# Optimization experiments

Hardware: AMD Instinct MI355X
Metric: run time of the kernel (lower is better)

Reference implementation:

```python
import jax, jax.numpy as jnp
import numpy as np

N = 20000      # nodes
E = 500000     # edges (~25 neighbors/node)
G = 64         # graphs in batch
NF = 64        # num_features (node dim)
NG = 100       # num_gaussians (edge dim)
L = 6          # conv layers
FC = 128       # fc_feat_size
NFC = 3        # num_fc_layers - 1
EMB = 92       # KHOT embedding width
CUTOFF = 6.0
EPS = 1e-5


def setup_inputs() -> dict:
    key = jax.random.key(0)
    ks = jax.random.split(key, 16)
    s = 0.05
    inp = {}
    inp['atomic_numbers'] = jax.random.randint(ks[0], (N,), 0, 100, dtype=jnp.int32)
    inp['neighbors_index'] = jax.random.randint(ks[1], (2, E), 0, N, dtype=jnp.int32)
    inp['distances'] = jax.random.uniform(ks[2], (E,), dtype=jnp.float32) * CUTOFF
    inp['batch'] = jnp.sort(jax.random.randint(ks[3], (N,), 0, G, dtype=jnp.int32))
    # parameters
    inp['embedding'] = jax.random.normal(ks[4], (100, EMB), jnp.float32) * s
    inp['nuc_W'] = jax.random.normal(ks[5], (EMB, NF), jnp.float32) * s
    inp['nuc_b'] = jnp.zeros((NF,), jnp.float32)
    inp['conv_W'] = jax.random.normal(ks[6], (L, 2 * NF + NG, 2 * NF), jnp.float32) * s
    inp['conv_b'] = jnp.zeros((L, 2 * NF), jnp.float32)
    inp['bn_g'] = jnp.ones((L, 2 * NF), jnp.float32)
    inp['bn_b'] = jnp.zeros((L, 2 * NF), jnp.float32)
    inp['ln_g'] = jnp.ones((L, NF), jnp.float32)
    inp['ln_b'] = jnp.zeros((L, NF), jnp.float32)
    inp['fc1_W'] = jax.random.normal(ks[7], (NF, FC), jnp.float32) * s
    inp['fc1_b'] = jnp.zeros((FC,), jnp.float32)
    inp['fcs_W'] = jax.random.normal(ks[8], (NFC, FC, FC), jnp.float32) * s
    inp['fcs_b'] = jnp.zeros((NFC, FC), jnp.float32)
    inp['out_W'] = jax.random.normal(ks[9], (FC, 1), jnp.float32) * s
    inp['out_b'] = jnp.zeros((1,), jnp.float32)
    return inp


def reference(atomic_numbers, neighbors_index, distances, batch,
              embedding, nuc_W, nuc_b, conv_W, conv_b, bn_g, bn_b,
              ln_g, ln_b, fc1_W, fc1_b, fcs_W, fcs_b, out_W, out_b):
    # Gaussian smearing of edge distances -> [E, NG]
    offsets = jnp.linspace(0.0, CUTOFF, NG)
    coeff = -0.5 / (offsets[1] - offsets[0]) ** 2
    ef = jnp.exp(coeff * (distances[:, None] - offsets) ** 2)

    # atom k-hot embedding -> nuclear linear embedding: [N, NF]
    x = embedding[atomic_numbers] @ nuc_W + nuc_b

    src, dst = neighbors_index[0], neighbors_index[1]  # x_j = src, x_i = dst

    for l in range(L):
        # edge message: gather + concat + linear
        z = jnp.concatenate([x[dst], x[src], ef], axis=1) @ conv_W[l] + conv_b[l]
        # BatchNorm1d over edges (training-mode batch statistics, biased var)
        mu = z.mean(axis=0)
        var = jnp.mean((z - mu) ** 2, axis=0)
        z = (z - mu) / jnp.sqrt(var + EPS) * bn_g[l] + bn_b[l]
        z1, z2 = jnp.split(z, 2, axis=1)
        m = jax.nn.sigmoid(z1) * jax.nn.softplus(z2)  # [E, NF]
        # scatter-add aggregate to target nodes
        agg = jax.ops.segment_sum(m, dst, num_segments=N)
        # LayerNorm + residual + softplus
        mu2 = agg.mean(axis=-1, keepdims=True)
        var2 = jnp.mean((agg - mu2) ** 2, axis=-1, keepdims=True)
        h = (agg - mu2) / jnp.sqrt(var2 + EPS) * ln_g[l] + ln_b[l]
        x = jax.nn.softplus(h + x)

    # mean pool per graph
    counts = jnp.maximum(jax.ops.segment_sum(jnp.ones((N,), x.dtype), batch, num_segments=G), 1.0)
    mol = jax.ops.segment_sum(x, batch, num_segments=G) / counts[:, None]

    h = jax.nn.softplus(mol @ fc1_W + fc1_b)
    for i in range(NFC):
        h = jax.nn.softplus(h @ fcs_W[i] + fcs_b[i])
    y = h @ out_W + out_b  # [G, 1]
    return y
```

## Files before the change

kernel.cpp:

```cpp
#include <hip/hip_runtime.h>
#include <hip/hip_fp16.h>
#include <cmath>

#define NN 20000
#define EE 500000
#define GG 64
#define TS 8192
#define SW 4096
#define EPS 1e-5f
#define LOG2E 1.442695040888963f
#define LN2 0.693147180559945f

typedef unsigned long long u64a __attribute__((aligned(4)));
typedef _Float16 f16x8 __attribute__((ext_vector_type(8)));
typedef float f32x4 __attribute__((ext_vector_type(4)));

__device__ __forceinline__ float softplus_ref(float x) {
    return fmaxf(x, 0.f) + log1pf(__expf(-fabsf(x)));
}
__device__ __forceinline__ float sigmoid_fast(float x) {
    return __builtin_amdgcn_rcpf(1.0f + __expf(-x));
}

__global__ void k_gtab(float* __restrict__ g) {
    int i = blockIdx.x * 256 + threadIdx.x;
    if (i >= TS * 100) return;
    int s = i / 100, k = i - 100 * s;
    float d = s * (6.0f / (TS - 1.0f));
    float o = k * (6.0f / 99.0f);
    float step = 6.0f / 99.0f;
    float coeff = -0.5f / (step * step);
    float df = d - o;
    g[i] = __expf(coeff * df * df);
}

__global__ void __launch_bounds__(256) k_build_T(
    const float* __restrict__ g, const float* __restrict__ convW,
    const float* __restrict__ convB, __half2* __restrict__ Tn) {
    int lane = threadIdx.x & 63;
    int wv = __builtin_amdgcn_readfirstlane(threadIdx.x >> 6);
    int l = blockIdx.y;
    int s0 = blockIdx.x * 16 + wv * 4;
    const float* w = convW + ((size_t)l * 228 + 128) * 128;
    const float* g0 = g + (size_t)s0 * 100;
    float b0 = convB[l * 128 + lane], b1 = convB[l * 128 + lane + 64];
    float2 a0 = {b0, b1}, a1 = {b0, b1}, a2 = {b0, b1}, a3 = {b0, b1};
#pragma unroll 4
    for (int k = 0; k < 100; k++) {
        float w0 = w[k * 128 + lane];
        float w1 = w[k * 128 + lane + 64];
        float ga = g0[k], gb = g0[100 + k], gc = g0[200 + k], gd = g0[300 + k];
        a0.x += ga * w0; a0.y += ga * w1;
        a1.x += gb * w0; a1.y += gb * w1;
        a2.x += gc * w0; a2.y += gc * w1;
        a3.x += gd * w0; a3.y += gd * w1;
    }
    Tn[((size_t)l * TS + s0 + 0) * 64 + lane] = __floats2half2_rn(a0.x, a0.y);
    Tn[((size_t)l * TS + s0 + 1) * 64 + lane] = __floats2half2_rn(a1.x, a1.y);
    Tn[((size_t)l * TS + s0 + 2) * 64 + lane] = __floats2half2_rn(a2.x, a2.y);
    Tn[((size_t)l * TS + s0 + 3) * 64 + lane] = __floats2half2_rn(a3.x, a3.y);
}

__global__ void k_prepW2(const float* __restrict__ convW, _Float16* __restrict__ Wf) {
    int lane = threadIdx.x;
    int ct = blockIdx.x;
    int half = blockIdx.y;
    int l = blockIdx.z;
    int p = ct * 16 + (lane & 15);
    int s = p >> 7;
    int r = p & 127;
    int colW = (r >> 1) + (r & 1) * 64;
    int k0 = half * 32 + (lane >> 4) * 8;
    _Float16* dst = Wf + (((size_t)(l * 16 + ct) * 2 + half) * 64 + lane) * 8;
#pragma unroll
    for (int i = 0; i < 8; i++) {
        float v = convW[((size_t)l * 228 + s * 64 + k0 + i) * 128 + colW];
        dst[i] = (_Float16)v;
    }
}

__global__ void k_embed(const int* __restrict__ an, const float* __restrict__ emb,
                        const float* __restrict__ W, const float* __restrict__ b,
                        float* __restrict__ x, _Float16* __restrict__ xh) {
    int c = threadIdx.x & 63, nl = threadIdx.x >> 6;
    int n = blockIdx.x * 4 + nl;
    if (n >= NN) return;
    const float* e = emb + (size_t)an[n] * 92;
    float acc = b[c];
#pragma unroll 4
    for (int k = 0; k < 92; k++) acc += e[k] * W[k * 64 + c];
    x[(size_t)n * 64 + c] = acc;
    xh[(size_t)n * 64 + c] = (_Float16)acc;
}

__global__ void k_hist(const int* __restrict__ dst, int* __restrict__ counts) {
    int e = blockIdx.x * 256 + threadIdx.x;
    if (e < EE) atomicAdd(&counts[dst[e]], 1);
}

__global__ void k_scan_local(const int* __restrict__ counts, int* __restrict__ rp,
                             int* __restrict__ bsum) {
    __shared__ int buf[1024];
    int b = blockIdx.x, tid = threadIdx.x;
    int i = b * 1024 + tid;
    int val = (i < NN) ? counts[i] : 0;
    buf[tid] = val;
    __syncthreads();
    for (int off = 1; off < 1024; off <<= 1) {
        int t = (tid >= off) ? buf[tid - off] : 0;
        __syncthreads();
        buf[tid] += t;
        __syncthreads();
    }
    if (i < NN) rp[i + 1] = buf[tid];
    if (tid == 1023) bsum[b] = buf[1023];
}

__global__ void k_scan_off(int* __restrict__ bsum, int nb) {
    if (threadIdx.x == 0) {
        int acc = 0;
        for (int b = 0; b < nb; b++) { int v = bsum[b]; bsum[b] = acc; acc += v; }
    }
}

__global__ void k_scan_add(int* __restrict__ rp, const int* __restrict__ bsum) {
    int b = blockIdx.x, tid = threadIdx.x;
    int i = b * 1024 + tid;
    if (i < NN) rp[i + 1] += bsum[b];
    if (b == 0 && tid == 0) rp[0] = 0;
}

__global__ void k_wsn(const int* __restrict__ rp, int* __restrict__ wsn) {
    int w = blockIdx.x * 256 + threadIdx.x;
    if (w >= SW) return;
    int e0 = (int)((long long)w * EE / SW);
    int lo = 0, hi = NN;
    while (lo + 1 < hi) {
        int mid = (lo + hi) >> 1;
        if (rp[mid] <= e0) lo = mid; else hi = mid;
    }
    wsn[w] = lo;
}

__global__ void k_scatter(const int* __restrict__ src, const int* __restrict__ dst,
                          const float* __restrict__ dist, const int* __restrict__ rp,
                          int* __restrict__ cursor, unsigned* __restrict__ ej) {
    int e = blockIdx.x * 256 + threadIdx.x;
    if (e < EE) {
        int d = dst[e];
        int p = atomicAdd(&cursor[d], 1);
        float t = dist[e] * ((TS - 1.0f) / 6.0f);
        int j = (int)(t + 0.5f);
        if (j > TS - 1) j = TS - 1;
        ej[rp[d] + p] = ((unsigned)src[e] << 13) | (unsigned)j;
    }
}

__global__ void __launch_bounds__(256) k_uvmm(
    const _Float16* __restrict__ xh, const _Float16* __restrict__ Wf, int l,
    _Float16* __restrict__ uph, _Float16* __restrict__ vph) {
    int lane = threadIdx.x & 63;
    int wv = threadIdx.x >> 6;
    int tile = blockIdx.x * 4 + wv;
    if (tile >= NN / 16) return;
    int node = tile * 16 + (lane & 15);
    const f16x8* ax = (const f16x8*)(xh + (size_t)node * 64 + ((lane >> 4) * 8));
    f16x8 a0 = ax[0];
    f16x8 a1 = ax[4];
    const f16x8* wf = (const f16x8*)Wf + (size_t)l * 16 * 2 * 64;
    int rowb = tile * 16 + ((lane >> 4) << 2);
#pragma unroll
    for (int ct = 0; ct < 16; ct++) {
        f16x8 b0 = wf[(ct * 2 + 0) * 64 + lane];
        f16x8 b1 = wf[(ct * 2 + 1) * 64 + lane];
        f32x4 acc = {0.f, 0.f, 0.f, 0.f};
        acc = __builtin_amdgcn_mfma_f32_16x16x32_f16(a0, b0, acc, 0, 0, 0);
        acc = __builtin_amdgcn_mfma_f32_16x16x32_f16(a1, b1, acc, 0, 0, 0);
        int p = ct * 16 + (lane & 15);
        _Float16* dst = (p < 128) ? (uph + p) : (vph + (p - 128));
#pragma unroll
        for (int r2 = 0; r2 < 4; r2++)
            dst[(size_t)(rowb + r2) * 128] = (_Float16)acc[r2];
    }
}

#define GRP2(P, BODY)                                                        \
    {                                                                        \
        unsigned e[P];                                                       \
        _Pragma("unroll")                                                    \
        for (int t = 0; t < P; t++) {                                        \
            unsigned long long ep = *(const u64a*)&ej[idx + 2 * t];          \
            e[t] = slot ? (unsigned)(ep >> 32) : (unsigned)ep;               \
        }                                                                    \
        __half2 vh[P], th[P];                                                \
        _Pragma("unroll")                                                    \
        for (int t = 0; t < P; t++) {                                        \
            vh[t] = vp[(size_t)(e[t] >> 13) * 64 + hp];                      \
            th[t] = Tn[(size_t)(e[t] & 8191u) * 64 + hp];                    \
        }                                                                    \
        _Pragma("unroll")                                                    \
        for (int t = 0; t < P; t++) { BODY }                                 \
    }

#define STATS_BODY                                                           \
    float2 vv = __half22float2(vh[t]);                                       \
    float2 tt = __half22float2(th[t]);                                       \
    float z0 = uu.x + vv.x + tt.x;                                           \
    float z1 = uu.y + vv.y + tt.y;                                           \
    sx += z0; qx += z0 * z0; sy += z1; qy += z1 * z1;

#define AGG_BODY                                                             \
    __half2 vt = __hadd2(vh[t], th[t]);                                      \
    float2 f = __half22float2(vt);                                           \
    float z0 = fmaf(A1, f.x, C1);                                            \
    float z1 = fmaf(A2, f.y, C2);                                            \
    float sg = __builtin_amdgcn_rcpf(1.0f + __builtin_amdgcn_exp2f(-z0));    \
    float sp = fmaxf(z1, 0.f) +                                              \
               __builtin_amdgcn_logf(1.0f + __builtin_amdgcn_exp2f(-fabsf(z1))); \
    acc += sg * sp;

__global__ void __launch_bounds__(256) k_stats_h(
    const __half2* __restrict__ up, const __half2* __restrict__ vp,
    const __half2* __restrict__ Tn, const unsigned* __restrict__ ej,
    const int* __restrict__ rp, const int* __restrict__ wsn,
    float* __restrict__ sums) {
    int lane = threadIdx.x & 63;
    int wv = __builtin_amdgcn_readfirstlane(threadIdx.x >> 6);
    int bid = blockIdx.x;
    int h = (bid >> 2) & 1;
    int r = ((bid >> 3) << 2) | (bid & 3);
    int slot = lane >> 5;
    int hp = h * 32 + (lane & 31);
    int w = r * 4 + wv;
    int e0 = (int)((long long)w * EE / SW);
    int e1 = (int)((long long)(w + 1) * EE / SW);
    int n = __builtin_amdgcn_readfirstlane(wsn[w]);
    int rend = __builtin_amdgcn_readfirstlane(rp[n + 1]);
    float sx = 0.f, sy = 0.f, qx = 0.f, qy = 0.f;
    int idx = e0;
    while (idx < e1) {
        while (idx >= rend) {
            ++n;
            rend = __builtin_amdgcn_readfirstlane(rp[n + 1]);
        }
        float2 uu = __half22float2(up[(size_t)n * 64 + hp]);
        int stop = (e1 < rend) ? e1 : rend;
        for (; idx + 16 <= stop; idx += 16) GRP2(8, STATS_BODY)
        if (idx + 8 <= stop) { GRP2(4, STATS_BODY) idx += 8; }
        if (idx + 4 <= stop) { GRP2(2, STATS_BODY) idx += 4; }
        if (idx + 2 <= stop) { GRP2(1, STATS_BODY) idx += 2; }
        if (idx < stop) {
            unsigned e = ej[idx];
            __half2 vh0 = vp[(size_t)(e >> 13) * 64 + hp];
            __half2 th0 = Tn[(size_t)(e & 8191u) * 64 + hp];
            float2 vv = __half22float2(vh0);
            float2 tt = __half22float2(th0);
            float z0 = uu.x + vv.x + tt.x;
            float z1 = uu.y + vv.y + tt.y;
            if (!slot) {
                sx += z0; qx += z0 * z0; sy += z1; qy += z1 * z1;
            }
            idx += 1;
        }
    }
    sx += __shfl_xor(sx, 32, 64); sy += __shfl_xor(sy, 32, 64);
    qx += __shfl_xor(qx, 32, 64); qy += __shfl_xor(qy, 32, 64);
    __shared__ float red[4][32][4];
    if (!slot) {
        float* rr = red[wv][lane & 31];
        rr[0] = sx; rr[1] = sy; rr[2] = qx; rr[3] = qy;
    }
    __syncthreads();
    if (wv == 0 && !slot) {
        for (int q = 1; q < 4; q++) {
            const float* rr = red[q][lane & 31];
            sx += rr[0]; sy += rr[1]; qx += rr[2]; qy += rr[3];
        }
        int c0 = hp;
        atomicAdd(&sums[c0], sx);
        atomicAdd(&sums[64 + c0], sy);
        atomicAdd(&sums[128 + c0], qx);
        atomicAdd(&sums[192 + c0], qy);
    }
}

__global__ void __launch_bounds__(256) k_aggh(
    const __half2* __restrict__ up, const __half2* __restrict__ vp,
    const __half2* __restrict__ Tn, const unsigned* __restrict__ ej,
    const int* __restrict__ rp, const float* __restrict__ sums,
    const float* __restrict__ bng, const float* __restrict__ bnb,
    int l, float* __restrict__ accbuf) {
    int lane = threadIdx.x & 63;
    int wv = __builtin_amdgcn_readfirstlane(threadIdx.x >> 6);
    int bid = blockIdx.x;
    int h = (bid >> 2) & 1;
    int r = ((bid >> 3) << 2) | (bid & 3);
    int slot = lane >> 5;
    int hp = h * 32 + (lane & 31);
    int i = r * 4 + wv;

    int c0 = hp;
    float mu1 = sums[c0] * (1.0f / EE);
    float var1 = sums[128 + c0] * (1.0f / EE) - mu1 * mu1;
    float A1 = rsqrtf(var1 + EPS) * bng[l * 128 + c0];
    float B1 = bnb[l * 128 + c0] - mu1 * A1;
    float mu2 = sums[64 + c0] * (1.0f / EE);
    float var2 = sums[192 + c0] * (1.0f / EE) - mu2 * mu2;
    float A2 = rsqrtf(var2 + EPS) * bng[l * 128 + 64 + c0];
    float B2 = bnb[l * 128 + 64 + c0] - mu2 * A2;

    float2 uu = __half22float2(up[(size_t)i * 64 + hp]);
    float C1 = fmaf(A1, uu.x, B1) * LOG2E;
    float C2 = fmaf(A2, uu.y, B2) * LOG2E;
    A1 *= LOG2E; A2 *= LOG2E;
    float acc = 0.f;
    int rs = __builtin_amdgcn_readfirstlane(rp[i]);
    int re = __builtin_amdgcn_readfirstlane(rp[i + 1]);
    int idx = rs;
    for (; idx + 16 <= re; idx += 16) GRP2(8, AGG_BODY)
    if (idx + 8 <= re) { GRP2(4, AGG_BODY) idx += 8; }
    if (idx + 4 <= re) { GRP2(2, AGG_BODY) idx += 4; }
    if (idx + 2 <= re) { GRP2(1, AGG_BODY) idx += 2; }
    if (idx < re) {
        unsigned e = ej[idx];
        __half2 vh0 = vp[(size_t)(e >> 13) * 64 + hp];
        __half2 th0 = Tn[(size_t)(e & 8191u) * 64 + hp];
        __half2 vt = __hadd2(vh0, th0);
        float2 f = __half22float2(vt);
        float z0 = fmaf(A1, f.x, C1);
        float z1 = fmaf(A2, f.y, C2);
        float sg = __builtin_amdgcn_rcpf(1.0f + __builtin_amdgcn_exp2f(-z0));
        float sp = fmaxf(z1, 0.f) +
                   __builtin_amdgcn_logf(1.0f + __builtin_amdgcn_exp2f(-fabsf(z1)));
        if (!slot) acc += sg * sp;
    }
    acc += __shfl_xor(acc, 32, 64);
    if (!slot) accbuf[(size_t)i * 64 + hp] = acc * LN2;
}

__global__ void __launch_bounds__(256) k_lnx(
    const float* __restrict__ accbuf,
    const float* __restrict__ lng, const float* __restrict__ lnb,
    int l, const float* __restrict__ xin, float* __restrict__ xout,
    _Float16* __restrict__ xh) {
    int lane = threadIdx.x & 63;
    int wv = __builtin_amdgcn_readfirstlane(threadIdx.x >> 6);
    int i = blockIdx.x * 4 + wv;
    float a = accbuf[(size_t)i * 64 + lane];
    float xr = xin[(size_t)i * 64 + lane];
    float s = a;
#pragma unroll
    for (int off = 32; off; off >>= 1) s += __shfl_xor(s, off, 64);
    float mean = s * (1.0f / 64.0f);
    float e0v = a - mean;
    float vv2 = e0v * e0v;
#pragma unroll
    for (int off = 32; off; off >>= 1) vv2 += __shfl_xor(vv2, off, 64);
    float var = vv2 * (1.0f / 64.0f);
    float h = e0v * rsqrtf(var + EPS) * lng[l * 64 + lane] + lnb[l * 64 + lane];
    float o = softplus_ref(h + xr);
    xout[(size_t)i * 64 + lane] = o;
    xh[(size_t)i * 64 + lane] = (_Float16)o;
}

__global__ void k_gp(const int* __restrict__ batch, int* __restrict__ gp) {
    int g = threadIdx.x;
    if (g > GG) return;
    int lo = 0, hi = NN;
    while (lo < hi) {
        int mid = (lo + hi) >> 1;
        if (batch[mid] < g) lo = mid + 1; else hi = mid;
    }
    gp[g] = lo;
}

__global__ void k_pool2(const float* __restrict__ x, const int* __restrict__ gp,
                        float* __restrict__ mols) {
    int g = blockIdx.x;
    int lane = threadIdx.x & 63, slot = threadIdx.x >> 6;
    int s0 = gp[g], s1 = gp[g + 1];
    float acc = 0.f;
    for (int n = s0 + slot; n < s1; n += 4) acc += x[(size_t)n * 64 + lane];
    __shared__ float red[4][64];
    red[slot][lane] = acc;
    __syncthreads();
    if (slot == 0) {
        float a = red[0][lane] + red[1][lane] + red[2][lane] + red[3][lane];
        float cc = fmaxf((float)(s1 - s0), 1.0f);
        mols[g * 64 + lane] = a / cc;
    }
}

__global__ void k_mlp(const float* __restrict__ mols,
                      const float* __restrict__ fc1W, const float* __restrict__ fc1b,
                      const float* __restrict__ fcsW, const float* __restrict__ fcsb,
                      const float* __restrict__ outW, const float* __restrict__ outb,
                      float* __restrict__ y) {
    int g = blockIdx.x, t = threadIdx.x;
    __shared__ float m[64];
    __shared__ float h[128];
    __shared__ float rbuf[128];
    if (t < 64) m[t] = mols[g * 64 + t];
    __syncthreads();
    float a = fc1b[t];
#pragma unroll 16
    for (int k = 0; k < 64; k++) a += m[k] * fc1W[k * 128 + t];
    h[t] = softplus_ref(a);
    __syncthreads();
    for (int i = 0; i < 3; i++) {
        float b = fcsb[i * 128 + t];
#pragma unroll 16
        for (int k = 0; k < 128; k++) b += h[k] * fcsW[((size_t)i * 128 + k) * 128 + t];
        __syncthreads();
        h[t] = softplus_ref(b);
        __syncthreads();
    }
    rbuf[t] = h[t] * outW[t];
    __syncthreads();
    if (t < 64) {
        float s2 = rbuf[t] + rbuf[t + 64];
#pragma unroll
        for (int off = 32; off; off >>= 1) s2 += __shfl_xor(s2, off, 64);
        if (t == 0) y[g] = s2 + outb[0];
    }
}

extern "C" void kernel_launch(void* const* d_in, const int* in_sizes, int n_in,
                              void* d_out, int out_size, void* d_ws, size_t ws_size,
                              hipStream_t stream) {
    const int*   an    = (const int*)d_in[0];
    const int*   nbr   = (const int*)d_in[1];
    const float* dist  = (const float*)d_in[2];
    const int*   batch = (const int*)d_in[3];
    const float* emb   = (const float*)d_in[4];
    const float* nucW  = (const float*)d_in[5];
    const float* nucB  = (const float*)d_in[6];
    const float* convW = (const float*)d_in[7];
    const float* convB = (const float*)d_in[8];
    const float* bng   = (const float*)d_in[9];
    const float* bnb   = (const float*)d_in[10];
    const float* lng   = (const float*)d_in[11];
    const float* lnb   = (const float*)d_in[12];
    const float* fc1W  = (const float*)d_in[13];
    const float* fc1b  = (const float*)d_in[14];
    const float* fcsW  = (const float*)d_in[15];
    const float* fcsb  = (const float*)d_in[16];
    const float* outW  = (const float*)d_in[17];
    const float* outb  = (const float*)d_in[18];
    const int* srcI = nbr;
    const int* dstI = nbr + EE;

    char* base = (char*)d_ws;
    size_t off = 0;
    auto alloc = [&](size_t b) { size_t r = off; off += (b + 255) & ~(size_t)255; return r; };
    float*     gtab   = (float*)(base + alloc((size_t)TS * 100 * 4));
    __half2*   Tall   = (__half2*)(base + alloc((size_t)6 * TS * 64 * 4));
    _Float16*  Wf     = (_Float16*)(base + alloc((size_t)6 * 16 * 2 * 64 * 8 * 2));
    float*     x0     = (float*)(base + alloc((size_t)NN * 64 * 4));
    float*     x1     = (float*)(base + alloc((size_t)NN * 64 * 4));
    _Float16*  xh     = (_Float16*)(base + alloc((size_t)NN * 64 * 2));
    _Float16*  uph    = (_Float16*)(base + alloc((size_t)NN * 128 * 2));
    _Float16*  vph    = (_Float16*)(base + alloc((size_t)NN * 128 * 2));
    float*     accb   = (float*)(base + alloc((size_t)NN * 64 * 4));
    float*     sums6  = (float*)(base + alloc((size_t)6 * 256 * 4));
    int*       counts = (int*)(base + alloc((size_t)NN * 4));
    int*       cursor = (int*)(base + alloc((size_t)NN * 4));
    int*       rp     = (int*)(base + alloc((size_t)(NN + 1) * 4));
    int*       bsum   = (int*)(base + alloc(64 * 4));
    unsigned*  ej     = (unsigned*)(base + alloc((size_t)(EE + 64) * 4));
    int*       wsn    = (int*)(base + alloc((size_t)SW * 4));
    float*     mols   = (float*)(base + alloc((size_t)GG * 64 * 4));
    int*       gp     = (int*)(base + alloc((size_t)(GG + 1) * 4));

    hipMemsetAsync(counts, 0, (size_t)NN * 4, stream);
    hipMemsetAsync(cursor, 0, (size_t)NN * 4, stream);
    hipMemsetAsync(sums6, 0, (size_t)6 * 256 * 4, stream);

    k_gtab<<<(TS * 100 + 255) / 256, 256, 0, stream>>>(gtab);
    k_build_T<<<dim3(TS / 16, 6), 256, 0, stream>>>(gtab, convW, convB, Tall);
    k_prepW2<<<dim3(16, 2, 6), 64, 0, stream>>>(convW, Wf);
    k_embed<<<(NN + 3) / 4, 256, 0, stream>>>(an, emb, nucW, nucB, x0, xh);
    k_hist<<<(EE + 255) / 256, 256, 0, stream>>>(dstI, counts);
    const int NB = (NN + 1023) / 1024;
    k_scan_local<<<NB, 1024, 0, stream>>>(counts, rp, bsum);
    k_scan_off<<<1, 64, 0, stream>>>(bsum, NB);
    k_scan_add<<<NB, 1024, 0, stream>>>(rp, bsum);
    k_wsn<<<SW / 256, 256, 0, stream>>>(rp, wsn);
    k_scatter<<<(EE + 255) / 256, 256, 0, stream>>>(srcI, dstI, dist, rp, cursor, ej);
    k_gp<<<1, 128, 0, stream>>>(batch, gp);

    float* xin = x0;
    float* xout = x1;
    const __half2* up = (const __half2*)uph;
    const __half2* vp = (const __half2*)vph;
    for (int l = 0; l < 6; l++) {
        k_uvmm<<<(NN / 16 + 3) / 4, 256, 0, stream>>>(xh, Wf, l, uph, vph);
        const __half2* Tnl = Tall + (size_t)l * TS * 64;
        float* sums = sums6 + (size_t)l * 256;
        k_stats_h<<<2048, 256, 0, stream>>>(up, vp, Tnl, ej, rp, wsn, sums);
        k_aggh<<<10000, 256, 0, stream>>>(up, vp, Tnl, ej, rp, sums,
                                          bng, bnb, l, accb);
        k_lnx<<<NN / 4, 256, 0, stream>>>(accb, lng, lnb, l, xin, xout, xh);
        float* tmp = xin; xin = xout; xout = tmp;
    }
    k_pool2<<<GG, 256, 0, stream>>>(xin, gp, mols);
    k_mlp<<<GG, 128, 0, stream>>>(mols, fc1W, fc1b, fcsW, fcsb, outW, outb, (float*)d_out);
}
```

Baseline: 747.0 us.

## Fuse LayerNorm into next-layer UV matmul and use FP8 stats for one layer

The LayerNorm+residual+softplus step is merged into the following layer's MFMA projection kernel, with a separate final LN kernel for the last layer. This removes the separate k_lnx pass and the xh half-precision round trip. Layer 3's BatchNorm statistics pass now reads FP8-scaled copies of v and the Gaussian table, built by an extra conversion kernel, to halve gather bytes. This adds a conversion launch and reduces the precision of that layer's statistics.

```diff
diff --git a/kernel.cpp b/kernel.cpp
--- a/kernel.cpp
+++ b/kernel.cpp
@@ -14,12 +14,10 @@
 typedef unsigned long long u64a __attribute__((aligned(4)));
 typedef _Float16 f16x8 __attribute__((ext_vector_type(8)));
 typedef float f32x4 __attribute__((ext_vector_type(4)));
+typedef float f32x2 __attribute__((ext_vector_type(2)));
 
 __device__ __forceinline__ float softplus_ref(float x) {
     return fmaxf(x, 0.f) + log1pf(__expf(-fabsf(x)));
-}
-__device__ __forceinline__ float sigmoid_fast(float x) {
-    return __builtin_amdgcn_rcpf(1.0f + __expf(-x));
 }
 
 __global__ void k_gtab(float* __restrict__ g) {
@@ -36,7 +34,8 @@
 
 __global__ void __launch_bounds__(256) k_build_T(
     const float* __restrict__ g, const float* __restrict__ convW,
-    const float* __restrict__ convB, __half2* __restrict__ Tn) {
+    const float* __restrict__ convB, __half2* __restrict__ Tn,
+    unsigned short* __restrict__ Tn8) {
     int lane = threadIdx.x & 63;
     int wv = __builtin_amdgcn_readfirstlane(threadIdx.x >> 6);
     int l = blockIdx.y;
@@ -59,6 +58,14 @@
     Tn[((size_t)l * TS + s0 + 1) * 64 + lane] = __floats2half2_rn(a1.x, a1.y);
     Tn[((size_t)l * TS + s0 + 2) * 64 + lane] = __floats2half2_rn(a2.x, a2.y);
     Tn[((size_t)l * TS + s0 + 3) * 64 + lane] = __floats2half2_rn(a3.x, a3.y);
+    int e0 = __builtin_amdgcn_cvt_pk_fp8_f32(16.f * a0.x, 16.f * a0.y, 0, false);
+    int e1 = __builtin_amdgcn_cvt_pk_fp8_f32(16.f * a1.x, 16.f * a1.y, 0, false);
+    int e2 = __builtin_amdgcn_cvt_pk_fp8_f32(16.f * a2.x, 16.f * a2.y, 0, false);
+    int e3 = __builtin_amdgcn_cvt_pk_fp8_f32(16.f * a3.x, 16.f * a3.y, 0, false);
+    Tn8[((size_t)l * TS + s0 + 0) * 64 + lane] = (unsigned short)(e0 & 0xffff);
+    Tn8[((size_t)l * TS + s0 + 1) * 64 + lane] = (unsigned short)(e1 & 0xffff);
+    Tn8[((size_t)l * TS + s0 + 2) * 64 + lane] = (unsigned short)(e2 & 0xffff);
+    Tn8[((size_t)l * TS + s0 + 3) * 64 + lane] = (unsigned short)(e3 & 0xffff);
 }
 
 __global__ void k_prepW2(const float* __restrict__ convW, _Float16* __restrict__ Wf) {
@@ -182,6 +189,83 @@
         for (int r2 = 0; r2 < 4; r2++)
             dst[(size_t)(rowb + r2) * 128] = (_Float16)acc[r2];
     }
+}
+
+__global__ void __launch_bounds__(256) k_uvln2(
+    const float* __restrict__ accb, const float* __restrict__ lng,
+    const float* __restrict__ lnb, int lp,
+    const float* __restrict__ xin, float* __restrict__ xout,
+    const _Float16* __restrict__ Wf, int l,
+    _Float16* __restrict__ uph, _Float16* __restrict__ vph) {
+    int lane = threadIdx.x & 63;
+    int wv = threadIdx.x >> 6;
+    int tile = blockIdx.x * 4 + wv;
+    if (tile >= NN / 16) return;
+    int node = tile * 16 + (lane & 15);
+    int ks = (lane >> 4) * 8;
+    const float* ab = accb + (size_t)node * 64;
+    const float* xb = xin + (size_t)node * 64;
+    float av[16], xr[16];
+#pragma unroll
+    for (int i = 0; i < 8; i++) { av[i] = ab[ks + i]; av[8 + i] = ab[32 + ks + i]; }
+#pragma unroll
+    for (int i = 0; i < 8; i++) { xr[i] = xb[ks + i]; xr[8 + i] = xb[32 + ks + i]; }
+    float s = 0.f;
+#pragma unroll
+    for (int i = 0; i < 16; i++) s += av[i];
+    s += __shfl_xor(s, 16, 64);
+    s += __shfl_xor(s, 32, 64);
+    float mean = s * (1.0f / 64.0f);
+    float vv = 0.f;
+#pragma unroll
+    for (int i = 0; i < 16; i++) { float d = av[i] - mean; vv += d * d; }
+    vv += __shfl_xor(vv, 16, 64);
+    vv += __shfl_xor(vv, 32, 64);
+    float rs = rsqrtf(vv * (1.0f / 64.0f) + EPS);
+    const float* lg = lng + lp * 64;
+    const float* lb = lnb + lp * 64;
+    f16x8 a0, a1;
+    float* xo = xout + (size_t)node * 64;
+#pragma unroll
+    for (int i = 0; i < 8; i++) {
+        float h = (av[i] - mean) * rs * lg[ks + i] + lb[ks + i];
+        float o = softplus_ref(h + xr[i]);
+        xo[ks + i] = o;
+        a0[i] = (_Float16)o;
+    }
+#pragma unroll
+    for (int i = 0; i < 8; i++) {
+        float h = (av[8 + i] - mean) * rs * lg[32 + ks + i] + lb[32 + ks + i];
+        float o = softplus_ref(h + xr[8 + i]);
+        xo[32 + ks + i] = o;
+        a1[i] = (_Float16)o;
+    }
+    const f16x8* wf = (const f16x8*)Wf + (size_t)l * 16 * 2 * 64;
+    int rowb = tile * 16 + ((lane >> 4) << 2);
+#pragma unroll
+    for (int ct = 0; ct < 16; ct++) {
+        f16x8 b0 = wf[(ct * 2 + 0) * 64 + lane];
+        f16x8 b1 = wf[(ct * 2 + 1) * 64 + lane];
+        f32x4 acc = {0.f, 0.f, 0.f, 0.f};
+        acc = __builtin_amdgcn_mfma_f32_16x16x32_f16(a0, b0, acc, 0, 0, 0);
+        acc = __builtin_amdgcn_mfma_f32_16x16x32_f16(a1, b1, acc, 0, 0, 0);
+        int p = ct * 16 + (lane & 15);
+        _Float16* dst = (p < 128) ? (uph + p) : (vph + (p - 128));
+#pragma unroll
+        for (int r2 = 0; r2 < 4; r2++)
+            dst[(size_t)(rowb + r2) * 128] = (_Float16)acc[r2];
+    }
+}
+
+__global__ void k_v8(const _Float16* __restrict__ vph, unsigned* __restrict__ vp8) {
+    int i = blockIdx.x * 256 + threadIdx.x;
+    if (i >= NN * 32) return;
+    uint2 hv = *(const uint2*)(vph + (size_t)i * 4);
+    float2 f0 = __half22float2(*(const __half2*)&hv.x);
+    float2 f1 = __half22float2(*(const __half2*)&hv.y);
+    int b = __builtin_amdgcn_cvt_pk_fp8_f32(16.f * f0.x, 16.f * f0.y, 0, false);
+    b = __builtin_amdgcn_cvt_pk_fp8_f32(16.f * f1.x, 16.f * f1.y, b, true);
+    vp8[i] = (unsigned)b;
 }
 
 #define GRP2(P, BODY)                                                        \
@@ -281,6 +365,110 @@
         atomicAdd(&sums[64 + c0], sy);
         atomicAdd(&sums[128 + c0], qx);
         atomicAdd(&sums[192 + c0], qy);
+    }
+}
+
+#define SGRP8B(P)                                                            \
+    {                                                                        \
+        unsigned e[P];                                                       \
+        _Pragma("unroll")                                                    \
+        for (int t = 0; t < P; t++) {                                        \
+            unsigned long long ep = *(const u64a*)&ej[idx + 2 * t];          \
+            e[t] = slot ? (unsigned)(ep >> 32) : (unsigned)ep;               \
+        }                                                                    \
+        unsigned vr[P], tr[P];                                               \
+        _Pragma("unroll")                                                    \
+        for (int t = 0; t < P; t++) {                                        \
+            vr[t] = vq8[(size_t)(e[t] >> 13) * 32 + q];                      \
+            tr[t] = tq8[(size_t)(e[t] & 8191u) * 32 + q];                    \
+        }                                                                    \
+        _Pragma("unroll")                                                    \
+        for (int t = 0; t < P; t++) {                                        \
+            f32x2 v0 = __builtin_amdgcn_cvt_pk_f32_fp8(vr[t], false);        \
+            f32x2 v1 = __builtin_amdgcn_cvt_pk_f32_fp8(vr[t], true);         \
+            f32x2 t0 = __builtin_amdgcn_cvt_pk_f32_fp8(tr[t], false);        \
+            f32x2 t1 = __builtin_amdgcn_cvt_pk_f32_fp8(tr[t], true);         \
+            float z0a = u0 + v0[0] + t0[0], z1a = u1 + v0[1] + t0[1];        \
+            float z0b = u2 + v1[0] + t1[0], z1b = u3 + v1[1] + t1[1];        \
+            sza += z0a; qza += z0a * z0a; sya += z1a; qya += z1a * z1a;      \
+            szb += z0b; qzb += z0b * z0b; syb += z1b; qyb += z1b * z1b;      \
+        }                                                                    \
+    }
+
+__global__ void __launch_bounds__(256) k_stats8b(
+    const __half2* __restrict__ up, const unsigned* __restrict__ vq8,
+    const unsigned* __restrict__ tq8, const unsigned* __restrict__ ej,
+    const int* __restrict__ rp, const int* __restrict__ wsn,
+    float* __restrict__ sums) {
+    int lane = threadIdx.x & 63;
+    int wv = __builtin_amdgcn_readfirstlane(threadIdx.x >> 6);
+    int slot = lane >> 5, q = lane & 31;
+    int w = blockIdx.x * 4 + wv;
+    int e0 = (int)((long long)w * EE / SW);
+    int e1 = (int)((long long)(w + 1) * EE / SW);
+    int n = __builtin_amdgcn_readfirstlane(wsn[w]);
+    int rend = __builtin_amdgcn_readfirstlane(rp[n + 1]);
+    float sza = 0, szb = 0, sya = 0, syb = 0;
+    float qza = 0, qzb = 0, qya = 0, qyb = 0;
+    float u0 = 0, u1 = 0, u2 = 0, u3 = 0;
+    int idx = e0;
+    while (idx < e1) {
+        while (idx >= rend) {
+            ++n;
+            rend = __builtin_amdgcn_readfirstlane(rp[n + 1]);
+        }
+        {
+            uint2 uw = *(const uint2*)&up[(size_t)n * 64 + 2 * q];
+            float2 fa = __half22float2(*(const __half2*)&uw.x);
+            float2 fb = __half22float2(*(const __half2*)&uw.y);
+            u0 = 16.0f * fa.x; u1 = 16.0f * fa.y;
+            u2 = 16.0f * fb.x; u3 = 16.0f * fb.y;
+        }
+        int stop = (e1 < rend) ? e1 : rend;
+        for (; idx + 16 <= stop; idx += 16) SGRP8B(8)
+        if (idx + 8 <= stop) { SGRP8B(4) idx += 8; }
+        if (idx + 4 <= stop) { SGRP8B(2) idx += 4; }
+        if (idx + 2 <= stop) { SGRP8B(1) idx += 2; }
+        if (idx < stop) {
+            unsigned e = ej[idx];
+            unsigned vr = vq8[(size_t)(e >> 13) * 32 + q];
+            unsigned tr = tq8[(size_t)(e & 8191u) * 32 + q];
+            f32x2 v0 = __builtin_amdgcn_cvt_pk_f32_fp8(vr, false);
+            f32x2 v1 = __builtin_amdgcn_cvt_pk_f32_fp8(vr, true);
+            f32x2 t0 = __builtin_amdgcn_cvt_pk_f32_fp8(tr, false);
+            f32x2 t1 = __builtin_amdgcn_cvt_pk_f32_fp8(tr, true);
+            float z0a = u0 + v0[0] + t0[0], z1a = u1 + v0[1] + t0[1];
+            float z0b = u2 + v1[0] + t1[0], z1b = u3 + v1[1] + t1[1];
+            if (!slot) {
+                sza += z0a; qza += z0a * z0a; sya += z1a; qya += z1a * z1a;
+                szb += z0b; qzb += z0b * z0b; syb += z1b; qyb += z1b * z1b;
+            }
+            idx += 1;
+        }
+    }
+    sza += __shfl_xor(sza, 32, 64); szb += __shfl_xor(szb, 32, 64);
+    sya += __shfl_xor(sya, 32, 64); syb += __shfl_xor(syb, 32, 64);
+    qza += __shfl_xor(qza, 32, 64); qzb += __shfl_xor(qzb, 32, 64);
+    qya += __shfl_xor(qya, 32, 64); qyb += __shfl_xor(qyb, 32, 64);
+    __shared__ float red[4][32][8];
+    if (!slot) {
+        float* rr = red[wv][q];
+        rr[0] = sza; rr[1] = szb; rr[2] = sya; rr[3] = syb;
+        rr[4] = qza; rr[5] = qzb; rr[6] = qya; rr[7] = qyb;
+    }
+    __syncthreads();
+    if (wv == 0 && !slot) {
+        for (int r = 1; r < 4; r++) {
+            const float* rr = red[r][q];
+            sza += rr[0]; szb += rr[1]; sya += rr[2]; syb += rr[3];
+            qza += rr[4]; qzb += rr[5]; qya += rr[6]; qyb += rr[7];
+        }
+        int cA = 2 * q, cB = 2 * q + 1;
+        const float s1 = 1.0f / 16.0f, s2 = 1.0f / 256.0f;
+        atomicAdd(&sums[cA], sza * s1);        atomicAdd(&sums[cB], szb * s1);
+        atomicAdd(&sums[64 + cA], sya * s1);   atomicAdd(&sums[64 + cB], syb * s1);
+        atomicAdd(&sums[128 + cA], qza * s2);  atomicAdd(&sums[128 + cB], qzb * s2);
+        atomicAdd(&sums[192 + cA], qya * s2);  atomicAdd(&sums[192 + cB], qyb * s2);
     }
 }
 
@@ -338,11 +526,10 @@
     if (!slot) accbuf[(size_t)i * 64 + hp] = acc * LN2;
 }
 
-__global__ void __launch_bounds__(256) k_lnx(
+__global__ void __launch_bounds__(256) k_lnfin(
     const float* __restrict__ accbuf,
     const float* __restrict__ lng, const float* __restrict__ lnb,
-    int l, const float* __restrict__ xin, float* __restrict__ xout,
-    _Float16* __restrict__ xh) {
+    int l, const float* __restrict__ xin, float* __restrict__ xout) {
     int lane = threadIdx.x & 63;
     int wv = __builtin_amdgcn_readfirstlane(threadIdx.x >> 6);
     int i = blockIdx.x * 4 + wv;
@@ -358,9 +545,7 @@
     for (int off = 32; off; off >>= 1) vv2 += __shfl_xor(vv2, off, 64);
     float var = vv2 * (1.0f / 64.0f);
     float h = e0v * rsqrtf(var + EPS) * lng[l * 64 + lane] + lnb[l * 64 + lane];
-    float o = softplus_ref(h + xr);
-    xout[(size_t)i * 64 + lane] = o;
-    xh[(size_t)i * 64 + lane] = (_Float16)o;
+    xout[(size_t)i * 64 + lane] = softplus_ref(h + xr);
 }
 
 __global__ void k_gp(const int* __restrict__ batch, int* __restrict__ gp) {
@@ -453,31 +638,33 @@
     char* base = (char*)d_ws;
     size_t off = 0;
     auto alloc = [&](size_t b) { size_t r = off; off += (b + 255) & ~(size_t)255; return r; };
-    float*     gtab   = (float*)(base + alloc((size_t)TS * 100 * 4));
-    __half2*   Tall   = (__half2*)(base + alloc((size_t)6 * TS * 64 * 4));
-    _Float16*  Wf     = (_Float16*)(base + alloc((size_t)6 * 16 * 2 * 64 * 8 * 2));
-    float*     x0     = (float*)(base + alloc((size_t)NN * 64 * 4));
-    float*     x1     = (float*)(base + alloc((size_t)NN * 64 * 4));
-    _Float16*  xh     = (_Float16*)(base + alloc((size_t)NN * 64 * 2));
-    _Float16*  uph    = (_Float16*)(base + alloc((size_t)NN * 128 * 2));
-    _Float16*  vph    = (_Float16*)(base + alloc((size_t)NN * 128 * 2));
-    float*     accb   = (float*)(base + alloc((size_t)NN * 64 * 4));
-    float*     sums6  = (float*)(base + alloc((size_t)6 * 256 * 4));
-    int*       counts = (int*)(base + alloc((size_t)NN * 4));
-    int*       cursor = (int*)(base + alloc((size_t)NN * 4));
-    int*       rp     = (int*)(base + alloc((size_t)(NN + 1) * 4));
-    int*       bsum   = (int*)(base + alloc(64 * 4));
-    unsigned*  ej     = (unsigned*)(base + alloc((size_t)(EE + 64) * 4));
-    int*       wsn    = (int*)(base + alloc((size_t)SW * 4));
-    float*     mols   = (float*)(base + alloc((size_t)GG * 64 * 4));
-    int*       gp     = (int*)(base + alloc((size_t)(GG + 1) * 4));
+    float*          gtab   = (float*)(base + alloc((size_t)TS * 100 * 4));
+    __half2*        Tall   = (__half2*)(base + alloc((size_t)6 * TS * 64 * 4));
+    unsigned short* Tall8  = (unsigned short*)(base + alloc((size_t)6 * TS * 64 * 2));
+    _Float16*       Wf     = (_Float16*)(base + alloc((size_t)6 * 16 * 2 * 64 * 8 * 2));
+    float*          x0     = (float*)(base + alloc((size_t)NN * 64 * 4));
+    float*          x1     = (float*)(base + alloc((size_t)NN * 64 * 4));
+    _Float16*       xh     = (_Float16*)(base + alloc((size_t)NN * 64 * 2));
+    _Float16*       uph    = (_Float16*)(base + alloc((size_t)NN * 128 * 2));
+    _Float16*       vph    = (_Float16*)(base + alloc((size_t)NN * 128 * 2));
+    unsigned*       vp8    = (unsigned*)(base + alloc((size_t)NN * 32 * 4));
+    float*          accb   = (float*)(base + alloc((size_t)NN * 64 * 4));
+    float*          sums6  = (float*)(base + alloc((size_t)6 * 256 * 4));
+    int*            counts = (int*)(base + alloc((size_t)NN * 4));
+    int*            cursor = (int*)(base + alloc((size_t)NN * 4));
+    int*            rp     = (int*)(base + alloc((size_t)(NN + 1) * 4));
+    int*            bsum   = (int*)(base + alloc(64 * 4));
+    unsigned*       ej     = (unsigned*)(base + alloc((size_t)(EE + 64) * 4));
+    int*            wsn    = (int*)(base + alloc((size_t)SW * 4));
+    float*          mols   = (float*)(base + alloc((size_t)GG * 64 * 4));
+    int*            gp     = (int*)(base + alloc((size_t)(GG + 1) * 4));
 
     hipMemsetAsync(counts, 0, (size_t)NN * 4, stream);
     hipMemsetAsync(cursor, 0, (size_t)NN * 4, stream);
     hipMemsetAsync(sums6, 0, (size_t)6 * 256 * 4, stream);
 
     k_gtab<<<(TS * 100 + 255) / 256, 256, 0, stream>>>(gtab);
-    k_build_T<<<dim3(TS / 16, 6), 256, 0, stream>>>(gtab, convW, convB, Tall);
+    k_build_T<<<dim3(TS / 16, 6), 256, 0, stream>>>(gtab, convW, convB, Tall, Tall8);
     k_prepW2<<<dim3(16, 2, 6), 64, 0, stream>>>(convW, Wf);
     k_embed<<<(NN + 3) / 4, 256, 0, stream>>>(an, emb, nucW, nucB, x0, xh);
     k_hist<<<(EE + 255) / 256, 256, 0, stream>>>(dstI, counts);
@@ -493,16 +680,28 @@
     float* xout = x1;
     const __half2* up = (const __half2*)uph;
     const __half2* vp = (const __half2*)vph;
+    const int UVB = (NN / 16 + 3) / 4;
     for (int l = 0; l < 6; l++) {
-        k_uvmm<<<(NN / 16 + 3) / 4, 256, 0, stream>>>(xh, Wf, l, uph, vph);
+        if (l == 0) {
+            k_uvmm<<<UVB, 256, 0, stream>>>(xh, Wf, 0, uph, vph);
+        } else {
+            k_uvln2<<<UVB, 256, 0, stream>>>(accb, lng, lnb, l - 1,
+                                             xin, xout, Wf, l, uph, vph);
+            float* tmp = xin; xin = xout; xout = tmp;
+        }
         const __half2* Tnl = Tall + (size_t)l * TS * 64;
         float* sums = sums6 + (size_t)l * 256;
-        k_stats_h<<<2048, 256, 0, stream>>>(up, vp, Tnl, ej, rp, wsn, sums);
+        if (l == 3) {
+            k_v8<<<(NN * 32 + 255) / 256, 256, 0, stream>>>(vph, vp8);
+            const unsigned* Tnl8 = (const unsigned*)(Tall8 + (size_t)l * TS * 64);
+            k_stats8b<<<1024, 256, 0, stream>>>(up, vp8, Tnl8, ej, rp, wsn, sums);
+        } else {
+            k_stats_h<<<2048, 256, 0, stream>>>(up, vp, Tnl, ej, rp, wsn, sums);
+        }
         k_aggh<<<10000, 256, 0, stream>>>(up, vp, Tnl, ej, rp, sums,
                                           bng, bnb, l, accb);
-        k_lnx<<<NN / 4, 256, 0, stream>>>(accb, lng, lnb, l, xin, xout, xh);
-        float* tmp = xin; xin = xout; xout = tmp;
-    }
-    k_pool2<<<GG, 256, 0, stream>>>(xin, gp, mols);
+    }
+    k_lnfin<<<NN / 4, 256, 0, stream>>>(accb, lng, lnb, 5, xin, xout);
+    k_pool2<<<GG, 256, 0, stream>>>(xout, gp, mols);
     k_mlp<<<GG, 128, 0, stream>>>(mols, fc1W, fc1b, fcsW, fcsb, outW, outb, (float*)d_out);
 }
```

New measurement: 770.4 us. 1.03x slower.
